# Kernel optimization log

Measured on AMD Instinct MI355X. Metric: run time of the kernel, lower is better.

The kernel has to match this reference:

```python
import jax, jax.numpy as jnp
import numpy as np

H = 128    # hidden_dim
B = 64     # batch (number of VRP instances)
N = 100    # nodes per instance
M = 2000   # moves per move-type per instance
SCALE = 0.02


def _gather_edges(e_emb, idx):
    # e_emb: [B, N, N, H]; idx: [B, M, K, 2] (i, j) -> [B, M, K, H]
    b = jnp.arange(e_emb.shape[0])[:, None, None]
    return e_emb[b, idx[..., 0], idx[..., 1]]


def _mlp1(x, W1, b1, W2, b2):
    # MLP(L=1): one hidden relu layer + linear output
    return jax.nn.relu(x @ W1 + b1) @ W2 + b2


def _action_net(x, W1, b1, W2, b2, W3, b3, Wo, bo):
    # MLP(L=3): three hidden relu layers + linear output to scalar logit
    h = jax.nn.relu(x @ W1 + b1)
    h = jax.nn.relu(h @ W2 + b2)
    h = jax.nn.relu(h @ W3 + b3)
    return h @ Wo + bo


def setup_inputs() -> dict:
    key = jax.random.key(0)
    ks = jax.random.split(key, 20)
    inp = {
        'e_emb': jax.random.normal(ks[0], (B, N, N, H), dtype=jnp.float32),
        'reloc_idx': jax.random.randint(ks[1], (B, M, 6, 2), 0, N),
        'cross_idx': jax.random.randint(ks[2], (B, M, 4, 2), 0, N),
        'twopt_idx': jax.random.randint(ks[3], (B, M, 4, 2), 0, N),
        # reloc_mlp: 6H -> H -> H
        'reloc_W1': jax.random.normal(ks[4], (6 * H, H), dtype=jnp.float32) * SCALE,
        'reloc_b1': jnp.zeros((H,), dtype=jnp.float32),
        'reloc_W2': jax.random.normal(ks[5], (H, H), dtype=jnp.float32) * SCALE,
        'reloc_b2': jnp.zeros((H,), dtype=jnp.float32),
        # cross_mlp (shared by cross and 2-opt): 4H -> H -> H
        'cross_W1': jax.random.normal(ks[6], (4 * H, H), dtype=jnp.float32) * SCALE,
        'cross_b1': jnp.zeros((H,), dtype=jnp.float32),
        'cross_W2': jax.random.normal(ks[7], (H, H), dtype=jnp.float32) * SCALE,
        'cross_b2': jnp.zeros((H,), dtype=jnp.float32),
        # action_net: H -> H -> H -> H -> 1
        'an_W1': jax.random.normal(ks[8], (H, H), dtype=jnp.float32) * SCALE,
        'an_b1': jnp.zeros((H,), dtype=jnp.float32),
        'an_W2': jax.random.normal(ks[9], (H, H), dtype=jnp.float32) * SCALE,
        'an_b2': jnp.zeros((H,), dtype=jnp.float32),
        'an_W3': jax.random.normal(ks[10], (H, H), dtype=jnp.float32) * SCALE,
        'an_b3': jnp.zeros((H,), dtype=jnp.float32),
        'an_Wo': jax.random.normal(ks[11], (H, 1), dtype=jnp.float32) * SCALE,
        'an_bo': jnp.zeros((1,), dtype=jnp.float32),
    }
    return inp


def reference(e_emb, reloc_idx, cross_idx, twopt_idx,
              reloc_W1, reloc_b1, reloc_W2, reloc_b2,
              cross_W1, cross_b1, cross_W2, cross_b2,
              an_W1, an_b1, an_W2, an_b2, an_W3, an_b3, an_Wo, an_bo):
    Bm, Mm = reloc_idx.shape[0], reloc_idx.shape[1]
    # embed_reloc_heuristic: gather 6 edge embeddings per relocate move, concat, MLP
    reloc_feat = _gather_edges(e_emb, reloc_idx).reshape(Bm, Mm, 6 * H)   # [B, M, 6H]
    reloc_emb = _mlp1(reloc_feat, reloc_W1, reloc_b1, reloc_W2, reloc_b2)  # [B, M, H]
    # embed_cross_heuristic for cross and 2-opt moves: 4 edges per move, shared cross_mlp
    cross_feat = _gather_edges(e_emb, cross_idx).reshape(Bm, Mm, 4 * H)
    cross_emb = _mlp1(cross_feat, cross_W1, cross_b1, cross_W2, cross_b2)
    twopt_feat = _gather_edges(e_emb, twopt_idx).reshape(Bm, Mm, 4 * H)
    twopt_emb = _mlp1(twopt_feat, cross_W1, cross_b1, cross_W2, cross_b2)
    # concat all moves per instance, score each with action_net
    all_moves = jnp.concatenate([reloc_emb, cross_emb, twopt_emb], axis=1)  # [B, 3M, H]
    logits = _action_net(all_moves, an_W1, an_b1, an_W2, an_b2, an_W3, an_b3, an_Wo, an_bo)
    return logits.squeeze(-1)  # [B, 3M] padded move logits
```

## Files before the change

### kernel.cpp

```cpp
#include <hip/hip_runtime.h>

#define H_  128
#define B_  64
#define N_  100
#define M_  2000
#define NT  512

#define RW1T 0
#define RW2T 196608
#define CW1T 229376
#define CW2T 360448
#define AW1T 393216
#define AW2T 425984
#define AW3T 458752
#define WIN_U 32768
#define PLANE_U 16384

typedef __attribute__((ext_vector_type(8)))  __bf16 bf16x8;
typedef __attribute__((ext_vector_type(16))) float  f32x16;

__device__ __forceinline__ unsigned short f2bf(float f) {
    unsigned int u = __float_as_uint(f);
    u = (u + 0x7FFFu + ((u >> 16) & 1u)) >> 16;
    return (unsigned short)u;
}
__device__ __forceinline__ float bf2f(unsigned short h) {
    return __uint_as_float(((unsigned int)h) << 16);
}

__global__ void __launch_bounds__(256)
wt_prep(const float* __restrict__ s0, const float* __restrict__ s1,
        const float* __restrict__ s2, const float* __restrict__ s3,
        const float* __restrict__ s4, const float* __restrict__ s5,
        const float* __restrict__ s6, unsigned short* __restrict__ wt)
{
    int g = blockIdx.x * 256 + threadIdx.x;
    if (g >= 245760) return;
    const float* src; int e, base;
    if      (g <  98304) { src = s0; e = g;          base = RW1T; }
    else if (g < 114688) { src = s1; e = g -  98304; base = RW2T; }
    else if (g < 180224) { src = s2; e = g - 114688; base = CW1T; }
    else if (g < 196608) { src = s3; e = g - 180224; base = CW2T; }
    else if (g < 212992) { src = s4; e = g - 196608; base = AW1T; }
    else if (g < 229376) { src = s5; e = g - 212992; base = AW2T; }
    else                 { src = s6; e = g - 229376; base = AW3T; }
    int k = e >> 7, n = e & 127;
    float v = src[e];
    unsigned short hi = f2bf(v);
    unsigned short lo = f2bf(v - bf2f(hi));
    int w  = k >> 7, kk = k & 127;
    size_t uoff = (size_t)base + (size_t)w * WIN_U
                + (size_t)((kk >> 3) * 128 + n) * 8 + (kk & 7);
    wt[uoff]           = hi;
    wt[uoff + PLANE_U] = lo;
}

__global__ void __launch_bounds__(NT, 4)
vrp_mfma(const float* __restrict__ e_emb,
         const int* __restrict__ reloc_idx, const int* __restrict__ cross_idx,
         const int* __restrict__ twopt_idx,
         const float* __restrict__ reloc_b1, const float* __restrict__ reloc_b2,
         const float* __restrict__ cross_b1, const float* __restrict__ cross_b2,
         const float* __restrict__ an_b1, const float* __restrict__ an_b2,
         const float* __restrict__ an_b3,
         const float* __restrict__ an_Wo, const float* __restrict__ an_bo,
         const unsigned short* __restrict__ wt,
         float* __restrict__ out)
{
    __shared__ __align__(16) unsigned short Ah[H_ * H_];
    __shared__ __align__(16) float bias_all[6 * H_];
    __shared__ float red[4 * H_];

    const int t = threadIdx.x;
    const int phys = blockIdx.x;
    const int virt = (phys & 7) * 384 + (phys >> 3);
    const int b    = virt / 48;
    const int rem  = virt - b * 48;
    const int type    = rem >> 4;
    const int blkTile = rem & 15;

    const int w    = t >> 6;
    const int l    = t & 63;
    const int l31  = l & 31;
    const int oct  = l >> 5;
    const int ntile = w & 3;
    const int mhalf = w >> 2;

    const int*  idxp = (type == 0) ? reloc_idx : (type == 1) ? cross_idx : twopt_idx;
    const int   KS   = (type == 0) ? 6 : 4;
    const int   w1t  = (type == 0) ? RW1T : CW1T;
    const int   w2t  = (type == 0) ? RW2T : CW2T;
    const float* b1p = (type == 0) ? reloc_b1 : cross_b1;
    const float* b2p = (type == 0) ? reloc_b2 : cross_b2;

    for (int i = t; i < 6 * H_; i += NT) {
        int g = i >> 7, ii = i & 127;
        const float* p = (g == 0) ? b1p : (g == 1) ? b2p : (g == 2) ? an_b1
                       : (g == 3) ? an_b2 : (g == 4) ? an_b3 : an_Wo;
        bias_all[i] = p[ii];
    }

    f32x16 acc0, acc1;
    #pragma unroll
    for (int i = 0; i < 16; ++i) { acc0[i] = 0.f; acc1[i] = 0.f; }

    auto zeroAcc = [&]() {
        #pragma unroll
        for (int i = 0; i < 16; ++i) { acc0[i] = 0.f; acc1[i] = 0.f; }
    };

    float4 vreg[8];
    auto loadA = [&](int s) {
        #pragma unroll
        for (int it = 0; it < 8; ++it) {
            int c = t + NT * it;
            int m = c >> 5, f4 = c & 31;
            int mg = blkTile * 128 + m; mg = (mg < M_) ? mg : (M_ - 1);
            const int* ip = idxp + (((b * M_ + mg) * KS + s) << 1);
            int ii = ip[0], jj = ip[1];
            vreg[it] = *((const float4*)(e_emb + (((size_t)b * N_ + ii) * N_ + jj) * H_) + f4);
        }
    };
    auto writeA = [&]() {
        #pragma unroll
        for (int it = 0; it < 8; ++it) {
            int c = t + NT * it;
            int m = c >> 5, f4 = c & 31;
            float4 v = vreg[it];
            uint2 hw;
            hw.x = f2bf(v.x) | ((unsigned)f2bf(v.y) << 16);
            hw.y = f2bf(v.z) | ((unsigned)f2bf(v.w) << 16);
            int off = m * 256 + ((f4 * 8) ^ ((m & 15) << 4));
            *(uint2*)((char*)Ah + off) = hw;
        }
    };

    auto runUnit = [&](const unsigned short* win) {
        const char* wph = (const char*)win;
        const int nrow  = ntile * 32 + l31;
        const int wbase = nrow * 16 + oct * 2048;
        const int mrow  = mhalf * 64 + l31;
        const int mbase = mrow * 256, Xm = (mrow & 15) << 4;
        bf16x8 cwh = *(const bf16x8*)(wph + wbase);
        #pragma unroll
        for (int ks = 0; ks < 8; ++ks) {
            bf16x8 nwh = cwh;
            if (ks < 7)
                nwh = *(const bf16x8*)(wph + wbase + (ks + 1) * 4096);
            int ka   = ks * 32 + oct * 16;
            int offA = mbase + (ka ^ Xm);
            bf16x8 a0 = *(const bf16x8*)((const char*)Ah + offA);
            bf16x8 a1 = *(const bf16x8*)((const char*)Ah + offA + 32 * 256);
            acc0 = __builtin_amdgcn_mfma_f32_32x32x16_bf16(cwh, a0, acc0, 0, 0, 0);
            acc1 = __builtin_amdgcn_mfma_f32_32x32x16_bf16(cwh, a1, acc1, 0, 0, 0);
            cwh = nwh;
        }
    };

    auto writeback = [&](int biasSlot, bool doRelu) {
        const float* bp = &bias_all[biasSlot * H_];
        #pragma unroll
        for (int tl = 0; tl < 2; ++tl) {
            int m  = mhalf * 64 + tl * 32 + l31;
            int mb = m * 256, Xm2 = (m & 15) << 4;
            #pragma unroll
            for (int q = 0; q < 4; ++q) {
                int n0 = ntile * 32 + q * 8 + oct * 4;
                float4 bq = *(const float4*)&bp[n0];
                float ba[4] = {bq.x, bq.y, bq.z, bq.w};
                unsigned short hs[4];
                #pragma unroll
                for (int r2 = 0; r2 < 4; ++r2) {
                    float v = (tl ? acc1[q * 4 + r2] : acc0[q * 4 + r2]) + ba[r2];
                    if (doRelu) v = fmaxf(v, 0.f);
                    hs[r2] = f2bf(v);
                }
                uint2 hw;
                hw.x = hs[0] | ((unsigned)hs[1] << 16);
                hw.y = hs[2] | ((unsigned)hs[3] << 16);
                int off = mb + ((n0 * 2) ^ Xm2);
                *(uint2*)((char*)Ah + off) = hw;
            }
        }
    };

    loadA(0);
    for (int s = 0; s < KS; ++s) {
        writeA();
        if (s + 1 < KS) loadA(s + 1);
        __syncthreads();
        runUnit(wt + w1t + s * WIN_U);
        __syncthreads();
    }
    writeback(0, true);  __syncthreads(); zeroAcc(); runUnit(wt + w2t);  __syncthreads();
    writeback(1, false); __syncthreads(); zeroAcc(); runUnit(wt + AW1T); __syncthreads();
    writeback(2, true);  __syncthreads(); zeroAcc(); runUnit(wt + AW2T); __syncthreads();
    writeback(3, true);  __syncthreads(); zeroAcc(); runUnit(wt + AW3T); __syncthreads();

    float p0 = 0.f, p1 = 0.f;
    {
        const float* b3p = &bias_all[4 * H_];
        const float* wop = &bias_all[5 * H_];
        #pragma unroll
        for (int q = 0; q < 4; ++q) {
            int n0 = ntile * 32 + q * 8 + oct * 4;
            float4 bq = *(const float4*)&b3p[n0];
            float4 wq = *(const float4*)&wop[n0];
            float ba[4] = {bq.x, bq.y, bq.z, bq.w};
            float wa[4] = {wq.x, wq.y, wq.z, wq.w};
            #pragma unroll
            for (int r2 = 0; r2 < 4; ++r2) {
                p0 += fmaxf(acc0[q * 4 + r2] + ba[r2], 0.f) * wa[r2];
                p1 += fmaxf(acc1[q * 4 + r2] + ba[r2], 0.f) * wa[r2];
            }
        }
    }
    p0 += __shfl_xor(p0, 32);
    p1 += __shfl_xor(p1, 32);
    if (l < 32) {
        red[ntile * H_ + mhalf * 64 + l31]      = p0;
        red[ntile * H_ + mhalf * 64 + 32 + l31] = p1;
    }
    __syncthreads();
    if (t < 128) {
        float sres = red[t] + red[H_ + t] + red[2 * H_ + t] + red[3 * H_ + t] + an_bo[0];
        int mg = blkTile * 128 + t;
        if (mg < M_)
            out[((size_t)(b * 3 + type)) * M_ + mg] = sres;
    }
}

extern "C" void kernel_launch(void* const* d_in, const int* in_sizes, int n_in,
                              void* d_out, int out_size, void* d_ws, size_t ws_size,
                              hipStream_t stream) {
    const float* e_emb     = (const float*)d_in[0];
    const int*   reloc_idx = (const int*)  d_in[1];
    const int*   cross_idx = (const int*)  d_in[2];
    const int*   twopt_idx = (const int*)  d_in[3];
    const float* reloc_W1  = (const float*)d_in[4];
    const float* reloc_b1  = (const float*)d_in[5];
    const float* reloc_W2  = (const float*)d_in[6];
    const float* reloc_b2  = (const float*)d_in[7];
    const float* cross_W1  = (const float*)d_in[8];
    const float* cross_b1  = (const float*)d_in[9];
    const float* cross_W2  = (const float*)d_in[10];
    const float* cross_b2  = (const float*)d_in[11];
    const float* an_W1     = (const float*)d_in[12];
    const float* an_b1     = (const float*)d_in[13];
    const float* an_W2     = (const float*)d_in[14];
    const float* an_b2     = (const float*)d_in[15];
    const float* an_W3     = (const float*)d_in[16];
    const float* an_b3     = (const float*)d_in[17];
    const float* an_Wo     = (const float*)d_in[18];
    const float* an_bo     = (const float*)d_in[19];
    float* out = (float*)d_out;
    unsigned short* wt = (unsigned short*)d_ws;

    hipLaunchKernelGGL(wt_prep, dim3(960), dim3(256), 0, stream,
                       reloc_W1, reloc_W2, cross_W1, cross_W2, an_W1, an_W2, an_W3, wt);
    hipLaunchKernelGGL(vrp_mfma, dim3(3 * B_ * 16), dim3(NT), 0, stream,
                       e_emb, reloc_idx, cross_idx, twopt_idx,
                       reloc_b1, reloc_b2, cross_b1, cross_b2,
                       an_b1, an_b2, an_b3, an_Wo, an_bo, wt, out);
}
```

Before: 199.8 us.

## Double the per-block move tile to 256 rows with 2x2 MFMA tiles per wave

Each block now handles 256 moves instead of 128, and each wave computes a 64x64 output patch with four accumulators rather than 64x32. Each weight fragment loaded from global memory is reused across twice as many rows, and the number of blocks is halved. The cost is a 64KB LDS activation buffer, which lowers the number of resident blocks per CU. The second half of each gather is also loaded synchronously instead of prefetched, so less memory latency is hidden.

```diff
diff --git a/kernel.cpp b/kernel.cpp
--- a/kernel.cpp
+++ b/kernel.cpp
@@ -5,6 +5,7 @@
 #define N_  100
 #define M_  2000
 #define NT  512
+#define TM  256
 
 #define RW1T 0
 #define RW2T 196608
@@ -67,24 +68,24 @@
          const unsigned short* __restrict__ wt,
          float* __restrict__ out)
 {
-    __shared__ __align__(16) unsigned short Ah[H_ * H_];
+    __shared__ __align__(16) unsigned short Ah[TM * H_];
     __shared__ __align__(16) float bias_all[6 * H_];
-    __shared__ float red[4 * H_];
+    __shared__ float red[2 * TM];
 
     const int t = threadIdx.x;
     const int phys = blockIdx.x;
-    const int virt = (phys & 7) * 384 + (phys >> 3);
-    const int b    = virt / 48;
-    const int rem  = virt - b * 48;
-    const int type    = rem >> 4;
-    const int blkTile = rem & 15;
+    const int virt = (phys & 7) * 192 + (phys >> 3);
+    const int b    = virt / 24;
+    const int rem  = virt - b * 24;
+    const int type    = rem >> 3;
+    const int blkTile = rem & 7;
 
     const int w    = t >> 6;
     const int l    = t & 63;
     const int l31  = l & 31;
     const int oct  = l >> 5;
-    const int ntile = w & 3;
-    const int mhalf = w >> 2;
+    const int nh   = w & 1;
+    const int mh   = w >> 1;
 
     const int*  idxp = (type == 0) ? reloc_idx : (type == 1) ? cross_idx : twopt_idx;
     const int   KS   = (type == 0) ? 6 : 4;
@@ -100,32 +101,31 @@
         bias_all[i] = p[ii];
     }
 
-    f32x16 acc0, acc1;
+    f32x16 acc00, acc01, acc10, acc11;
     #pragma unroll
-    for (int i = 0; i < 16; ++i) { acc0[i] = 0.f; acc1[i] = 0.f; }
-
+    for (int i = 0; i < 16; ++i) { acc00[i] = 0.f; acc01[i] = 0.f; acc10[i] = 0.f; acc11[i] = 0.f; }
     auto zeroAcc = [&]() {
         #pragma unroll
-        for (int i = 0; i < 16; ++i) { acc0[i] = 0.f; acc1[i] = 0.f; }
+        for (int i = 0; i < 16; ++i) { acc00[i] = 0.f; acc01[i] = 0.f; acc10[i] = 0.f; acc11[i] = 0.f; }
     };
 
     float4 vreg[8];
-    auto loadA = [&](int s) {
+    auto loadA = [&](int s, int half) {
         #pragma unroll
         for (int it = 0; it < 8; ++it) {
             int c = t + NT * it;
             int m = c >> 5, f4 = c & 31;
-            int mg = blkTile * 128 + m; mg = (mg < M_) ? mg : (M_ - 1);
+            int mg = blkTile * TM + half * 128 + m; mg = (mg < M_) ? mg : (M_ - 1);
             const int* ip = idxp + (((b * M_ + mg) * KS + s) << 1);
             int ii = ip[0], jj = ip[1];
             vreg[it] = *((const float4*)(e_emb + (((size_t)b * N_ + ii) * N_ + jj) * H_) + f4);
         }
     };
-    auto writeA = [&]() {
+    auto writeA = [&](int half) {
         #pragma unroll
         for (int it = 0; it < 8; ++it) {
             int c = t + NT * it;
-            int m = c >> 5, f4 = c & 31;
+            int m = half * 128 + (c >> 5), f4 = c & 31;
             float4 v = vreg[it];
             uint2 hw;
             hw.x = f2bf(v.x) | ((unsigned)f2bf(v.y) << 16);
@@ -134,60 +134,87 @@
             *(uint2*)((char*)Ah + off) = hw;
         }
     };
+    auto directA = [&](int s, int half) {
+        #pragma unroll
+        for (int it = 0; it < 8; ++it) {
+            int c = t + NT * it;
+            int m = c >> 5, f4 = c & 31;
+            int mg = blkTile * TM + half * 128 + m; mg = (mg < M_) ? mg : (M_ - 1);
+            const int* ip = idxp + (((b * M_ + mg) * KS + s) << 1);
+            int ii = ip[0], jj = ip[1];
+            float4 v = *((const float4*)(e_emb + (((size_t)b * N_ + ii) * N_ + jj) * H_) + f4);
+            uint2 hw;
+            hw.x = f2bf(v.x) | ((unsigned)f2bf(v.y) << 16);
+            hw.y = f2bf(v.z) | ((unsigned)f2bf(v.w) << 16);
+            int mm = half * 128 + m;
+            int off = mm * 256 + ((f4 * 8) ^ ((mm & 15) << 4));
+            *(uint2*)((char*)Ah + off) = hw;
+        }
+    };
 
     auto runUnit = [&](const unsigned short* win) {
         const char* wph = (const char*)win;
-        const int nrow  = ntile * 32 + l31;
-        const int wbase = nrow * 16 + oct * 2048;
-        const int mrow  = mhalf * 64 + l31;
-        const int mbase = mrow * 256, Xm = (mrow & 15) << 4;
-        bf16x8 cwh = *(const bf16x8*)(wph + wbase);
+        const int wb0 = (nh * 64 + l31) * 16 + oct * 2048;
+        const int wb1 = wb0 + 32 * 16;
+        const int mrow0 = mh * 64 + l31, mrow1 = mrow0 + 32;
+        const int mb0 = mrow0 * 256, Xm0 = (mrow0 & 15) << 4;
+        const int mb1 = mrow1 * 256, Xm1 = (mrow1 & 15) << 4;
+        bf16x8 cw0 = *(const bf16x8*)(wph + wb0);
+        bf16x8 cw1 = *(const bf16x8*)(wph + wb1);
         #pragma unroll
         for (int ks = 0; ks < 8; ++ks) {
-            bf16x8 nwh = cwh;
-            if (ks < 7)
-                nwh = *(const bf16x8*)(wph + wbase + (ks + 1) * 4096);
-            int ka   = ks * 32 + oct * 16;
-            int offA = mbase + (ka ^ Xm);
-            bf16x8 a0 = *(const bf16x8*)((const char*)Ah + offA);
-            bf16x8 a1 = *(const bf16x8*)((const char*)Ah + offA + 32 * 256);
-            acc0 = __builtin_amdgcn_mfma_f32_32x32x16_bf16(cwh, a0, acc0, 0, 0, 0);
-            acc1 = __builtin_amdgcn_mfma_f32_32x32x16_bf16(cwh, a1, acc1, 0, 0, 0);
-            cwh = nwh;
+            bf16x8 nw0 = cw0, nw1 = cw1;
+            if (ks < 7) {
+                nw0 = *(const bf16x8*)(wph + wb0 + (ks + 1) * 4096);
+                nw1 = *(const bf16x8*)(wph + wb1 + (ks + 1) * 4096);
+            }
+            int ka = ks * 32 + oct * 16;
+            bf16x8 a0 = *(const bf16x8*)((const char*)Ah + mb0 + (ka ^ Xm0));
+            bf16x8 a1 = *(const bf16x8*)((const char*)Ah + mb1 + (ka ^ Xm1));
+            acc00 = __builtin_amdgcn_mfma_f32_32x32x16_bf16(cw0, a0, acc00, 0, 0, 0);
+            acc01 = __builtin_amdgcn_mfma_f32_32x32x16_bf16(cw0, a1, acc01, 0, 0, 0);
+            acc10 = __builtin_amdgcn_mfma_f32_32x32x16_bf16(cw1, a0, acc10, 0, 0, 0);
+            acc11 = __builtin_amdgcn_mfma_f32_32x32x16_bf16(cw1, a1, acc11, 0, 0, 0);
+            cw0 = nw0; cw1 = nw1;
         }
     };
 
     auto writeback = [&](int biasSlot, bool doRelu) {
         const float* bp = &bias_all[biasSlot * H_];
         #pragma unroll
-        for (int tl = 0; tl < 2; ++tl) {
-            int m  = mhalf * 64 + tl * 32 + l31;
+        for (int mi = 0; mi < 2; ++mi) {
+            int m  = mh * 64 + mi * 32 + l31;
             int mb = m * 256, Xm2 = (m & 15) << 4;
             #pragma unroll
-            for (int q = 0; q < 4; ++q) {
-                int n0 = ntile * 32 + q * 8 + oct * 4;
-                float4 bq = *(const float4*)&bp[n0];
-                float ba[4] = {bq.x, bq.y, bq.z, bq.w};
-                unsigned short hs[4];
+            for (int ni = 0; ni < 2; ++ni) {
+                const f32x16& A = mi ? (ni ? acc11 : acc01) : (ni ? acc10 : acc00);
                 #pragma unroll
-                for (int r2 = 0; r2 < 4; ++r2) {
-                    float v = (tl ? acc1[q * 4 + r2] : acc0[q * 4 + r2]) + ba[r2];
-                    if (doRelu) v = fmaxf(v, 0.f);
-                    hs[r2] = f2bf(v);
+                for (int q = 0; q < 4; ++q) {
+                    int n0 = nh * 64 + ni * 32 + q * 8 + oct * 4;
+                    float4 bq = *(const float4*)&bp[n0];
+                    float ba[4] = {bq.x, bq.y, bq.z, bq.w};
+                    unsigned short hs[4];
+                    #pragma unroll
+                    for (int r2 = 0; r2 < 4; ++r2) {
+                        float v = A[q * 4 + r2] + ba[r2];
+                        if (doRelu) v = fmaxf(v, 0.f);
+                        hs[r2] = f2bf(v);
+                    }
+                    uint2 hw;
+                    hw.x = hs[0] | ((unsigned)hs[1] << 16);
+                    hw.y = hs[2] | ((unsigned)hs[3] << 16);
+                    int off = mb + ((n0 * 2) ^ Xm2);
+                    *(uint2*)((char*)Ah + off) = hw;
                 }
-                uint2 hw;
-                hw.x = hs[0] | ((unsigned)hs[1] << 16);
-                hw.y = hs[2] | ((unsigned)hs[3] << 16);
-                int off = mb + ((n0 * 2) ^ Xm2);
-                *(uint2*)((char*)Ah + off) = hw;
             }
         }
     };
 
-    loadA(0);
+    loadA(0, 0);
     for (int s = 0; s < KS; ++s) {
-        writeA();
-        if (s + 1 < KS) loadA(s + 1);
+        writeA(0);
+        directA(s, 1);
+        if (s + 1 < KS) loadA(s + 1, 0);
         __syncthreads();
         runUnit(wt + w1t + s * WIN_U);
         __syncthreads();
@@ -197,34 +224,39 @@
     writeback(2, true);  __syncthreads(); zeroAcc(); runUnit(wt + AW2T); __syncthreads();
     writeback(3, true);  __syncthreads(); zeroAcc(); runUnit(wt + AW3T); __syncthreads();
 
-    float p0 = 0.f, p1 = 0.f;
     {
         const float* b3p = &bias_all[4 * H_];
         const float* wop = &bias_all[5 * H_];
-        #pragma unroll
-        for (int q = 0; q < 4; ++q) {
-            int n0 = ntile * 32 + q * 8 + oct * 4;
-            float4 bq = *(const float4*)&b3p[n0];
-            float4 wq = *(const float4*)&wop[n0];
-            float ba[4] = {bq.x, bq.y, bq.z, bq.w};
-            float wa[4] = {wq.x, wq.y, wq.z, wq.w};
+        float p0 = 0.f, p1 = 0.f;
+        #pragma unroll
+        for (int ni = 0; ni < 2; ++ni) {
             #pragma unroll
-            for (int r2 = 0; r2 < 4; ++r2) {
-                p0 += fmaxf(acc0[q * 4 + r2] + ba[r2], 0.f) * wa[r2];
-                p1 += fmaxf(acc1[q * 4 + r2] + ba[r2], 0.f) * wa[r2];
+            for (int q = 0; q < 4; ++q) {
+                int n0 = nh * 64 + ni * 32 + q * 8 + oct * 4;
+                float4 bq = *(const float4*)&b3p[n0];
+                float4 wq = *(const float4*)&wop[n0];
+                float ba[4] = {bq.x, bq.y, bq.z, bq.w};
+                float wa[4] = {wq.x, wq.y, wq.z, wq.w};
+                const f32x16& A0 = ni ? acc10 : acc00;
+                const f32x16& A1 = ni ? acc11 : acc01;
+                #pragma unroll
+                for (int r2 = 0; r2 < 4; ++r2) {
+                    p0 += fmaxf(A0[q * 4 + r2] + ba[r2], 0.f) * wa[r2];
+                    p1 += fmaxf(A1[q * 4 + r2] + ba[r2], 0.f) * wa[r2];
+                }
             }
         }
-    }
-    p0 += __shfl_xor(p0, 32);
-    p1 += __shfl_xor(p1, 32);
-    if (l < 32) {
-        red[ntile * H_ + mhalf * 64 + l31]      = p0;
-        red[ntile * H_ + mhalf * 64 + 32 + l31] = p1;
+        p0 += __shfl_xor(p0, 32);
+        p1 += __shfl_xor(p1, 32);
+        if (l < 32) {
+            red[nh * TM + mh * 64 + l31]      = p0;
+            red[nh * TM + mh * 64 + 32 + l31] = p1;
+        }
     }
     __syncthreads();
-    if (t < 128) {
-        float sres = red[t] + red[H_ + t] + red[2 * H_ + t] + red[3 * H_ + t] + an_bo[0];
-        int mg = blkTile * 128 + t;
+    if (t < TM) {
+        float sres = red[t] + red[TM + t] + an_bo[0];
+        int mg = blkTile * TM + t;
         if (mg < M_)
             out[((size_t)(b * 3 + type)) * M_ + mg] = sres;
     }
@@ -258,7 +290,7 @@
 
     hipLaunchKernelGGL(wt_prep, dim3(960), dim3(256), 0, stream,
                        reloc_W1, reloc_W2, cross_W1, cross_W2, an_W1, an_W2, an_W3, wt);
-    hipLaunchKernelGGL(vrp_mfma, dim3(3 * B_ * 16), dim3(NT), 0, stream,
+    hipLaunchKernelGGL(vrp_mfma, dim3(3 * B_ * 8), dim3(NT), 0, stream,
                        e_emb, reloc_idx, cross_idx, twopt_idx,
                        reloc_b1, reloc_b2, cross_b1, cross_b2,
                        an_b1, an_b2, an_b3, an_Wo, an_bo, wt, out);
```

Measured after the change: 386.7 us. +93.5%, slower.
